# Optimization experiments

Measured on AMD Instinct MI355X. Metric: run time of the kernel, lower is better.

Reference implementation:

```python
import jax, jax.numpy as jnp
import numpy as np

N_NODES = 100000
N_EDGES = 1600000
IN_FEATS = 128
HIDDEN = 128


def _graph_conv(x, W, b, src, dst, n_nodes):
    # DGL GraphConv with norm='both': out = D_in^{-1/2} * A^T * (D_out^{-1/2} * x) @ W + b
    ones = jnp.ones((src.shape[0],), dtype=x.dtype)
    deg_out = jax.ops.segment_sum(ones, src, num_segments=n_nodes)
    deg_in = jax.ops.segment_sum(ones, dst, num_segments=n_nodes)
    norm_src = jax.lax.rsqrt(jnp.clip(deg_out, 1.0))  # [N]
    norm_dst = jax.lax.rsqrt(jnp.clip(deg_in, 1.0))   # [N]
    h = x @ W                                          # [N, F_out]
    msg = h[src] * norm_src[src][:, None]              # gather by edge src: [E, F_out]
    agg = jax.ops.segment_sum(msg, dst, num_segments=n_nodes)  # scatter-add to dst
    return agg * norm_dst[:, None] + b


def setup_inputs() -> dict:
    key = jax.random.key(0)
    ks = jax.random.split(key, 9)
    x = jax.random.normal(ks[0], (N_NODES, IN_FEATS), dtype=jnp.float32)
    src = jax.random.randint(ks[1], (N_EDGES,), 0, N_NODES, dtype=jnp.int32)
    dst = jax.random.randint(ks[2], (N_EDGES,), 0, N_NODES, dtype=jnp.int32)
    s1 = 1.0 / np.sqrt(IN_FEATS)
    s2 = 1.0 / np.sqrt(HIDDEN)
    W1 = jax.random.uniform(ks[3], (IN_FEATS, HIDDEN), jnp.float32, -s1, s1)
    b1 = jnp.zeros((HIDDEN,), jnp.float32)
    W2 = jax.random.uniform(ks[4], (HIDDEN, HIDDEN), jnp.float32, -s2, s2)
    b2 = jnp.zeros((HIDDEN,), jnp.float32)
    sp = 1.0 / np.sqrt(2 * HIDDEN)
    Wp = jax.random.uniform(ks[5], (2 * HIDDEN, 1), jnp.float32, -sp, sp)
    bp = jax.random.uniform(ks[6], (1,), jnp.float32, -sp, sp)
    return {"x": x, "W1": W1, "b1": b1, "W2": W2, "b2": b2,
            "Wp": Wp, "bp": bp, "src": src, "dst": dst}


def reference(x, W1, b1, W2, b2, Wp, bp, src, dst):
    n_nodes = x.shape[0]
    h = _graph_conv(x, W1, b1, src, dst, n_nodes)
    h = jax.nn.relu(h)
    h = _graph_conv(h, W2, b2, src, dst, n_nodes)  # final node embeddings [N, H]
    # predict_links on the same edge list: cat(h[u], h[v]) -> linear -> sigmoid
    edge_h = jnp.concatenate([h[src], h[dst]], axis=1)  # [E, 2H]
    scores = jax.nn.sigmoid(edge_h @ Wp + bp)           # [E, 1]
    return scores
```

## Files before the change

kernel.cpp:

```cpp
#include <hip/hip_runtime.h>
#include <cstdint>
#include <cstddef>

#define NN 100000
#define NE 1600000
#define F  128
#define NPAD 100352
#define NBUCK 782
#define BCAPG 2560
#define CHUNK 3125

typedef __attribute__((ext_vector_type(8))) short bf16x8;
typedef __attribute__((ext_vector_type(4))) float f32x4;

__device__ __forceinline__ unsigned short f2bf(float f) {
    unsigned u = __float_as_uint(f);
    unsigned r = (u + 0x7fffu + ((u >> 16) & 1u)) >> 16;
    return (unsigned short)r;
}
__device__ __forceinline__ void acc_bf8s(const uint4 v, const float ns, float* acc) {
    acc[0] += __uint_as_float(v.x << 16) * ns;
    acc[1] += __uint_as_float(v.x & 0xffff0000u) * ns;
    acc[2] += __uint_as_float(v.y << 16) * ns;
    acc[3] += __uint_as_float(v.y & 0xffff0000u) * ns;
    acc[4] += __uint_as_float(v.z << 16) * ns;
    acc[5] += __uint_as_float(v.z & 0xffff0000u) * ns;
    acc[6] += __uint_as_float(v.w << 16) * ns;
    acc[7] += __uint_as_float(v.w & 0xffff0000u) * ns;
}
__device__ __forceinline__ float deg2norm(int d) {
    return rsqrtf((float)max(d, 1));
}

__global__ void setup_kernel(const float* __restrict__ W2, const float* __restrict__ Wp,
                             const float* __restrict__ b2, const float* __restrict__ bp,
                             float* __restrict__ consts, float2* __restrict__ V) {
    const int tid = threadIdx.x;
    if (tid < 128) {
        float sa = 0.f, sc = 0.f;
        #pragma unroll 8
        for (int j = 0; j < F; ++j) {
            const float w = W2[tid * F + j];
            sa += w * Wp[j];
            sc += w * Wp[F + j];
        }
        V[tid] = make_float2(sa, sc);
    } else if (tid < 192) {
        const int l = tid - 128;
        const float2 bb = *(const float2*)&b2[2 * l];
        const float2 wa = *(const float2*)&Wp[2 * l];
        const float2 wc = *(const float2*)&Wp[F + 2 * l];
        float s = bb.x * (wa.x + wc.x) + bb.y * (wa.y + wc.y);
        #pragma unroll
        for (int m = 32; m > 0; m >>= 1) s += __shfl_xor(s, m);
        if (l == 0) consts[0] = s + bp[0];
    }
}

__global__ __launch_bounds__(256, 3)
void gemm1_fill_kernel(const float* __restrict__ in, const float* __restrict__ W,
                       unsigned short* __restrict__ out_bf,
                       const int* __restrict__ src, const int* __restrict__ dst,
                       int* __restrict__ deg_out, int* __restrict__ gCur,
                       int* __restrict__ srcPart) {
    __shared__ __align__(16) char smem[25008];

    const int g = blockIdx.x;
    const int r3 = g % 3;
    const int tid = threadIdx.x;

    if (r3 != 0) {
        int* packedL = (int*)smem;
        unsigned short* bktL = (unsigned short*)(packedL + CHUNK);
        int* hist = (int*)(smem + 18752);
        int* curL = hist + NBUCK;
        const int fid = (g / 3) * 2 + (r3 - 1);
        const int e0 = fid * CHUNK;
        const int nCh = min(CHUNK, NE - e0);
        for (int i = tid; i < NBUCK; i += 256) hist[i] = 0;
        __syncthreads();
        for (int i = tid; i < nCh; i += 256) {
            const int s = src[e0 + i];
            const int d = dst[e0 + i];
            atomicAdd(&deg_out[s], 1);
            const int bkt = d >> 7;
            atomicAdd(&hist[bkt], 1);
            packedL[i] = s | ((d & 127) << 17);
            bktL[i] = (unsigned short)bkt;
        }
        __syncthreads();
        for (int b = tid; b < NBUCK; b += 256) {
            const int c = hist[b];
            curL[b] = (c > 0) ? (b * BCAPG + atomicAdd(&gCur[b], c)) : 0;
        }
        __syncthreads();
        for (int i = tid; i < nCh; i += 256) {
            const int bkt = bktL[i];
            const int p = atomicAdd(&curL[bkt], 1);
            if (p < (bkt + 1) * BCAPG)
                srcPart[p] = packedL[i];
        }
        return;
    }

    char* A_s = smem;

    const int gid  = g / 3;
    const int w    = tid >> 6;
    const int lane = tid & 63;
    const int ml   = lane & 15;
    const int quad = lane >> 4;

    bf16x8 Bf[4][2];
    #pragma unroll
    for (int kb = 0; kb < 4; ++kb) {
        #pragma unroll
        for (int nb = 0; nb < 2; ++nb) {
            const int n = 32 * w + nb * 16 + ml;
            const int k0 = kb * 32 + quad * 8;
            #pragma unroll
            for (int j = 0; j < 8; ++j)
                Bf[kb][nb][j] = (short)f2bf(W[(k0 + j) * F + n]);
        }
    }

    const int nTiles = NN / 32;
    for (int tile = gid; tile < nTiles; tile += 256) {
        const int row0 = tile * 32;
        __syncthreads();
        #pragma unroll
        for (int c = 0; c < 2; ++c) {
            const int i2 = tid + 256 * c;
            const int m  = i2 >> 4;
            const int o  = i2 & 15;
            const float* xr = &in[(size_t)(row0 + m) * F + o * 8];
            const float4 v0 = *(const float4*)xr;
            const float4 v1 = *(const float4*)(xr + 4);
            short h8[8];
            h8[0] = (short)f2bf(v0.x); h8[1] = (short)f2bf(v0.y);
            h8[2] = (short)f2bf(v0.z); h8[3] = (short)f2bf(v0.w);
            h8[4] = (short)f2bf(v1.x); h8[5] = (short)f2bf(v1.y);
            h8[6] = (short)f2bf(v1.z); h8[7] = (short)f2bf(v1.w);
            const int kb2 = o >> 2, q2 = o & 3, ml2 = m & 15, mh2 = m >> 4;
            const int fo = (((mh2 * 4 + kb2) * 64) + q2 * 16 + ml2) * 16;
            *(bf16x8*)(A_s + fo) = *(bf16x8*)h8;
        }
        __syncthreads();

        f32x4 acc00 = {0,0,0,0}, acc01 = {0,0,0,0}, acc10 = {0,0,0,0}, acc11 = {0,0,0,0};
        #pragma unroll
        for (int kb = 0; kb < 4; ++kb) {
            const bf16x8 ah0 = *(const bf16x8*)(A_s + (kb * 64 + lane) * 16);
            const bf16x8 ah1 = *(const bf16x8*)(A_s + ((4 + kb) * 64 + lane) * 16);
            acc00 = __builtin_amdgcn_mfma_f32_16x16x32_bf16(ah0, Bf[kb][0], acc00, 0, 0, 0);
            acc01 = __builtin_amdgcn_mfma_f32_16x16x32_bf16(ah0, Bf[kb][1], acc01, 0, 0, 0);
            acc10 = __builtin_amdgcn_mfma_f32_16x16x32_bf16(ah1, Bf[kb][0], acc10, 0, 0, 0);
            acc11 = __builtin_amdgcn_mfma_f32_16x16x32_bf16(ah1, Bf[kb][1], acc11, 0, 0, 0);
        }

        #pragma unroll
        for (int mh = 0; mh < 2; ++mh) {
            #pragma unroll
            for (int nb = 0; nb < 2; ++nb) {
                const f32x4 a = (mh == 0) ? (nb == 0 ? acc00 : acc01)
                                          : (nb == 0 ? acc10 : acc11);
                const int row = row0 + mh * 16 + quad * 4;
                const int col = 32 * w + nb * 16 + ml;
                #pragma unroll
                for (int r = 0; r < 4; ++r)
                    out_bf[(size_t)(row + r) * F + col] = f2bf(a[r]);
            }
        }
    }
}

__global__ __launch_bounds__(256)
void gather_sort_kernel(const unsigned short* __restrict__ hs,
                        int* __restrict__ srcPart, const int* __restrict__ gCur,
                        const int* __restrict__ deg_out, const float* __restrict__ bias,
                        const float2* __restrict__ V, float2* __restrict__ uw,
                        int* __restrict__ offs, int* __restrict__ ends,
                        float* __restrict__ norm_dst) {
    __shared__ int cnt[128];
    __shared__ int loc[128];
    __shared__ int cur[128];
    __shared__ int sortedL[BCAPG];

    const int b   = blockIdx.x;
    const int tid = threadIdx.x;
    const int nlo = b * 128;
    const int nCnt = min(128, NN - nlo);
    const int eBase = b * BCAPG;
    const int total = min(gCur[b], BCAPG);

    if (tid < 128) cnt[tid] = 0;
    __syncthreads();
    for (int i = tid; i < total; i += 256)
        atomicAdd(&cnt[(srcPart[eBase + i] >> 17) & 127], 1);
    __syncthreads();
    if (tid < 128) loc[tid] = cnt[tid];
    __syncthreads();
    for (int off = 1; off < 128; off <<= 1) {
        int v = 0;
        if (tid < 128 && tid >= off) v = loc[tid - off];
        __syncthreads();
        if (tid < 128) loc[tid] += v;
        __syncthreads();
    }
    if (tid < 128) cur[tid] = loc[tid] - cnt[tid];
    if (tid < nCnt) {
        const int st = eBase + loc[tid] - cnt[tid];
        offs[nlo + tid] = st;
        ends[nlo + tid] = st + cnt[tid];
        norm_dst[nlo + tid] = deg2norm(cnt[tid]);
    }
    __syncthreads();
    for (int i = tid; i < total; i += 256) {
        const int v = srcPart[eBase + i];
        const int r = atomicAdd(&cur[(v >> 17) & 127], 1);
        sortedL[r] = v & 0x1FFFF;
    }
    __syncthreads();
    for (int i = tid; i < total; i += 256)
        srcPart[eBase + i] = sortedL[i];

    const int w  = tid >> 6;
    const int l  = tid & 63;
    const int q  = l >> 4;
    const int c8 = (l & 15) * 8;
    float bb[8];
    *(float4*)&bb[0] = *(const float4*)&bias[c8];
    *(float4*)&bb[4] = *(const float4*)&bias[c8 + 4];
    float2 Vl[8];
    #pragma unroll
    for (int k = 0; k < 8; ++k) Vl[k] = V[c8 + k];

    const int nhEnd = min((w + 1) * 32, nCnt);
    for (int nh = w * 32; nh < nhEnd; ++nh) {
        const int end = loc[nh];
        const int beg = end - cnt[nh];
        float acc[8] = {0.f, 0.f, 0.f, 0.f, 0.f, 0.f, 0.f, 0.f};
        int j = beg;
        for (; j + 16 <= end; j += 16) {
            const int s0 = sortedL[j + q];
            const int s1 = sortedL[j + 4 + q];
            const int s2 = sortedL[j + 8 + q];
            const int s3 = sortedL[j + 12 + q];
            const float ns0 = deg2norm(deg_out[s0]);
            const float ns1 = deg2norm(deg_out[s1]);
            const float ns2 = deg2norm(deg_out[s2]);
            const float ns3 = deg2norm(deg_out[s3]);
            const uint4 v0 = *(const uint4*)&hs[(size_t)s0 * F + c8];
            const uint4 v1 = *(const uint4*)&hs[(size_t)s1 * F + c8];
            const uint4 v2 = *(const uint4*)&hs[(size_t)s2 * F + c8];
            const uint4 v3 = *(const uint4*)&hs[(size_t)s3 * F + c8];
            acc_bf8s(v0, ns0, acc);
            acc_bf8s(v1, ns1, acc);
            acc_bf8s(v2, ns2, acc);
            acc_bf8s(v3, ns3, acc);
        }
        for (; j + 8 <= end; j += 8) {
            const int s0 = sortedL[j + q];
            const int s1 = sortedL[j + 4 + q];
            const float ns0 = deg2norm(deg_out[s0]);
            const float ns1 = deg2norm(deg_out[s1]);
            const uint4 v0 = *(const uint4*)&hs[(size_t)s0 * F + c8];
            const uint4 v1 = *(const uint4*)&hs[(size_t)s1 * F + c8];
            acc_bf8s(v0, ns0, acc);
            acc_bf8s(v1, ns1, acc);
        }
        for (; j + 4 <= end; j += 4) {
            const int s = sortedL[j + q];
            const float ns = deg2norm(deg_out[s]);
            const uint4 v = *(const uint4*)&hs[(size_t)s * F + c8];
            acc_bf8s(v, ns, acc);
        }
        if (j + q < end) {
            const int s = sortedL[j + q];
            const float ns = deg2norm(deg_out[s]);
            const uint4 v = *(const uint4*)&hs[(size_t)s * F + c8];
            acc_bf8s(v, ns, acc);
        }
        #pragma unroll
        for (int k = 0; k < 8; ++k) {
            acc[k] += __shfl_xor(acc[k], 16);
            acc[k] += __shfl_xor(acc[k], 32);
        }

        const int n = nlo + nh;
        const float nd = deg2norm(cnt[nh]);
        float pa = 0.f, pc = 0.f;
        #pragma unroll
        for (int k = 0; k < 8; ++k) {
            const float ok = fmaxf(acc[k] * nd + bb[k], 0.f);
            pa += ok * Vl[k].x;
            pc += ok * Vl[k].y;
        }
        #pragma unroll
        for (int m = 1; m <= 8; m <<= 1) {
            pa += __shfl_xor(pa, m);
            pc += __shfl_xor(pc, m);
        }
        if (l == 0) {
            const float ns = deg2norm(deg_out[n]);
            uw[n] = make_float2(ns * pa, ns * pc);
        }
    }
}

__global__ void ac_kernel(const float2* __restrict__ uw, const int* __restrict__ sorted_src,
                          const int* __restrict__ offs, const int* __restrict__ ends,
                          const float* __restrict__ norm_dst,
                          float* __restrict__ A, float* __restrict__ C, int nN) {
    const int gid = blockIdx.x * blockDim.x + threadIdx.x;
    const int n   = gid >> 3;
    if (n >= nN) return;
    const int sub = gid & 7;
    const int beg = offs[n];
    const int end = ends[n];
    float su = 0.f, sw = 0.f;
    for (int j = beg + sub; j < end; j += 8) {
        const float2 t = uw[sorted_src[j]];
        su += t.x;
        sw += t.y;
    }
    su += __shfl_xor(su, 1); sw += __shfl_xor(sw, 1);
    su += __shfl_xor(su, 2); sw += __shfl_xor(sw, 2);
    su += __shfl_xor(su, 4); sw += __shfl_xor(sw, 4);
    if (sub == 0) {
        const float nd = norm_dst[n];
        A[n] = nd * su;
        C[n] = nd * sw;
    }
}

__global__ void score_kernel(const float* __restrict__ A, const float* __restrict__ C,
                             const int4* __restrict__ src4, const int4* __restrict__ dst4,
                             const float* __restrict__ consts, float4* __restrict__ out4,
                             int nE4) {
    const int i = blockIdx.x * blockDim.x + threadIdx.x;
    if (i < nE4) {
        const int4 s = src4[i];
        const int4 d = dst4[i];
        const float cc = consts[0];
        float4 o;
        o.x = 1.f / (1.f + __expf(-(A[s.x] + C[d.x] + cc)));
        o.y = 1.f / (1.f + __expf(-(A[s.y] + C[d.y] + cc)));
        o.z = 1.f / (1.f + __expf(-(A[s.z] + C[d.z] + cc)));
        o.w = 1.f / (1.f + __expf(-(A[s.w] + C[d.w] + cc)));
        out4[i] = o;
    }
}

extern "C" void kernel_launch(void* const* d_in, const int* in_sizes, int n_in,
                              void* d_out, int out_size, void* d_ws, size_t ws_size,
                              hipStream_t stream) {
    const float* x  = (const float*)d_in[0];
    const float* W1 = (const float*)d_in[1];
    const float* b1 = (const float*)d_in[2];
    const float* W2 = (const float*)d_in[3];
    const float* b2 = (const float*)d_in[4];
    const float* Wp = (const float*)d_in[5];
    const float* bp = (const float*)d_in[6];
    const int*   src = (const int*)d_in[7];
    const int*   dst = (const int*)d_in[8];
    float* out = (float*)d_out;

    float* ws        = (float*)d_ws;
    float* bufA      = ws;
    int*   gCur      = (int*)(ws + NPAD);
    float* bufC      = ws + NPAD + 1024;
    float* norm_dst  = bufC + NPAD;
    int*   offs      = (int*)(norm_dst + NPAD);
    int*   ends      = offs + NPAD;
    float* consts    = (float*)(ends + NPAD);
    float2* V        = (float2*)(consts + 16);
    float2* uw       = V + 128;
    int*   srcPart   = (int*)(uw + NN);
    unsigned short* hs_bf = (unsigned short*)(srcPart + (size_t)NBUCK * BCAPG);

    hipMemsetAsync(bufA, 0, (NPAD + 1024) * sizeof(int), stream);
    setup_kernel<<<1, 256, 0, stream>>>(W2, Wp, b2, bp, consts, V);

    gemm1_fill_kernel<<<768, 256, 0, stream>>>(x, W1, hs_bf, src, dst,
                                               (int*)bufA, gCur, srcPart);

    gather_sort_kernel<<<NBUCK, 256, 0, stream>>>(hs_bf, srcPart, gCur, (const int*)bufA, b1,
                                                  V, uw, offs, ends, norm_dst);

    ac_kernel<<<(NN * 8 + 255) / 256, 256, 0, stream>>>(uw, srcPart, offs, ends, norm_dst,
                                                        bufA, bufC, NN);

    score_kernel<<<(NE / 4 + 255) / 256, 256, 0, stream>>>(bufA, bufC, (const int4*)src,
                                                           (const int4*)dst, consts,
                                                           (float4*)out, NE / 4);
}
```

Measured before the change: 312.9 us.

## Aggregate raw bf16 features first, then apply W1 GEMM per destination bucket

Reorders layer 1 so neighbour features are aggregated before the W1 multiply: the first kernel now only casts x to bf16 (plus edge bucketing and the setup constants, merged in as extra blocks). The gather kernel stages the aggregated 128 rows per bucket in shared memory and runs the MFMA GEMM with W1 there before the fused ReLU/projection. This removes the separate GEMM pass and one kernel launch. In exchange, each gather block reloads and converts W1 from global memory and uses 32KB more LDS, which may lower occupancy.

```diff
diff --git a/kernel.cpp b/kernel.cpp
--- a/kernel.cpp
+++ b/kernel.cpp
@@ -8,7 +8,8 @@
 #define NPAD 100352
 #define NBUCK 782
 #define BCAPG 2560
-#define CHUNK 3125
+#define FILLB 1024
+#define CHUNK 1563
 
 typedef __attribute__((ext_vector_type(8))) short bf16x8;
 typedef __attribute__((ext_vector_type(4))) float f32x4;
@@ -32,159 +33,112 @@
     return rsqrtf((float)max(d, 1));
 }
 
-__global__ void setup_kernel(const float* __restrict__ W2, const float* __restrict__ Wp,
-                             const float* __restrict__ b2, const float* __restrict__ bp,
-                             float* __restrict__ consts, float2* __restrict__ V) {
+__global__ __launch_bounds__(256, 3)
+void cast_fill_kernel(const float* __restrict__ x, unsigned short* __restrict__ xb,
+                      const int* __restrict__ src, const int* __restrict__ dst,
+                      int* __restrict__ deg_out, int* __restrict__ gCur,
+                      int* __restrict__ srcPart,
+                      const float* __restrict__ W2, const float* __restrict__ Wp,
+                      const float* __restrict__ b2, const float* __restrict__ bp,
+                      float* __restrict__ consts, float2* __restrict__ V) {
+    __shared__ __align__(16) char smem[15664];
+    const int g = blockIdx.x;
     const int tid = threadIdx.x;
-    if (tid < 128) {
-        float sa = 0.f, sc = 0.f;
-        #pragma unroll 8
-        for (int j = 0; j < F; ++j) {
-            const float w = W2[tid * F + j];
-            sa += w * Wp[j];
-            sc += w * Wp[F + j];
-        }
-        V[tid] = make_float2(sa, sc);
-    } else if (tid < 192) {
-        const int l = tid - 128;
-        const float2 bb = *(const float2*)&b2[2 * l];
-        const float2 wa = *(const float2*)&Wp[2 * l];
-        const float2 wc = *(const float2*)&Wp[F + 2 * l];
-        float s = bb.x * (wa.x + wc.x) + bb.y * (wa.y + wc.y);
-        #pragma unroll
-        for (int m = 32; m > 0; m >>= 1) s += __shfl_xor(s, m);
-        if (l == 0) consts[0] = s + bp[0];
-    }
-}
-
-__global__ __launch_bounds__(256, 3)
-void gemm1_fill_kernel(const float* __restrict__ in, const float* __restrict__ W,
-                       unsigned short* __restrict__ out_bf,
-                       const int* __restrict__ src, const int* __restrict__ dst,
-                       int* __restrict__ deg_out, int* __restrict__ gCur,
-                       int* __restrict__ srcPart) {
-    __shared__ __align__(16) char smem[25008];
-
-    const int g = blockIdx.x;
-    const int r3 = g % 3;
-    const int tid = threadIdx.x;
-
-    if (r3 != 0) {
-        int* packedL = (int*)smem;
-        unsigned short* bktL = (unsigned short*)(packedL + CHUNK);
-        int* hist = (int*)(smem + 18752);
-        int* curL = hist + NBUCK;
-        const int fid = (g / 3) * 2 + (r3 - 1);
-        const int e0 = fid * CHUNK;
-        const int nCh = min(CHUNK, NE - e0);
-        for (int i = tid; i < NBUCK; i += 256) hist[i] = 0;
-        __syncthreads();
-        for (int i = tid; i < nCh; i += 256) {
-            const int s = src[e0 + i];
-            const int d = dst[e0 + i];
-            atomicAdd(&deg_out[s], 1);
-            const int bkt = d >> 7;
-            atomicAdd(&hist[bkt], 1);
-            packedL[i] = s | ((d & 127) << 17);
-            bktL[i] = (unsigned short)bkt;
-        }
-        __syncthreads();
-        for (int b = tid; b < NBUCK; b += 256) {
-            const int c = hist[b];
-            curL[b] = (c > 0) ? (b * BCAPG + atomicAdd(&gCur[b], c)) : 0;
-        }
-        __syncthreads();
-        for (int i = tid; i < nCh; i += 256) {
-            const int bkt = bktL[i];
-            const int p = atomicAdd(&curL[bkt], 1);
-            if (p < (bkt + 1) * BCAPG)
-                srcPart[p] = packedL[i];
+
+    if (g >= 1152) {
+        const int i = g - 1152;
+        if (i < 128) {
+            float* red = (float*)smem;
+            float pa = 0.f, pc = 0.f;
+            if (tid < 128) {
+                const float wv = W2[i * F + tid];
+                pa = wv * Wp[tid];
+                pc = wv * Wp[F + tid];
+            }
+            #pragma unroll
+            for (int m = 32; m > 0; m >>= 1) {
+                pa += __shfl_xor(pa, m);
+                pc += __shfl_xor(pc, m);
+            }
+            if (tid < 128 && (tid & 63) == 0) {
+                red[(tid >> 6) * 2]     = pa;
+                red[(tid >> 6) * 2 + 1] = pc;
+            }
+            __syncthreads();
+            if (tid == 0) V[i] = make_float2(red[0] + red[2], red[1] + red[3]);
+        } else if (tid < 64) {
+            const float2 bb = *(const float2*)&b2[2 * tid];
+            const float2 wa = *(const float2*)&Wp[2 * tid];
+            const float2 wc = *(const float2*)&Wp[F + 2 * tid];
+            float s = bb.x * (wa.x + wc.x) + bb.y * (wa.y + wc.y);
+            #pragma unroll
+            for (int m = 32; m > 0; m >>= 1) s += __shfl_xor(s, m);
+            if (tid == 0) consts[0] = s + bp[0];
         }
         return;
     }
 
-    char* A_s = smem;
-
-    const int gid  = g / 3;
-    const int w    = tid >> 6;
-    const int lane = tid & 63;
-    const int ml   = lane & 15;
-    const int quad = lane >> 4;
-
-    bf16x8 Bf[4][2];
-    #pragma unroll
-    for (int kb = 0; kb < 4; ++kb) {
-        #pragma unroll
-        for (int nb = 0; nb < 2; ++nb) {
-            const int n = 32 * w + nb * 16 + ml;
-            const int k0 = kb * 32 + quad * 8;
-            #pragma unroll
-            for (int j = 0; j < 8; ++j)
-                Bf[kb][nb][j] = (short)f2bf(W[(k0 + j) * F + n]);
-        }
-    }
-
-    const int nTiles = NN / 32;
-    for (int tile = gid; tile < nTiles; tile += 256) {
-        const int row0 = tile * 32;
-        __syncthreads();
-        #pragma unroll
-        for (int c = 0; c < 2; ++c) {
-            const int i2 = tid + 256 * c;
-            const int m  = i2 >> 4;
-            const int o  = i2 & 15;
-            const float* xr = &in[(size_t)(row0 + m) * F + o * 8];
-            const float4 v0 = *(const float4*)xr;
-            const float4 v1 = *(const float4*)(xr + 4);
+    const int r9 = g % 9;
+    if (r9 == 4) {
+        const int cb = g / 9;
+        const int total8 = NN * F / 8;
+        for (int i = cb * 256 + tid; i < total8; i += 128 * 256) {
+            const float4 v0 = *(const float4*)&x[(size_t)i * 8];
+            const float4 v1 = *(const float4*)&x[(size_t)i * 8 + 4];
             short h8[8];
             h8[0] = (short)f2bf(v0.x); h8[1] = (short)f2bf(v0.y);
             h8[2] = (short)f2bf(v0.z); h8[3] = (short)f2bf(v0.w);
             h8[4] = (short)f2bf(v1.x); h8[5] = (short)f2bf(v1.y);
             h8[6] = (short)f2bf(v1.z); h8[7] = (short)f2bf(v1.w);
-            const int kb2 = o >> 2, q2 = o & 3, ml2 = m & 15, mh2 = m >> 4;
-            const int fo = (((mh2 * 4 + kb2) * 64) + q2 * 16 + ml2) * 16;
-            *(bf16x8*)(A_s + fo) = *(bf16x8*)h8;
-        }
-        __syncthreads();
-
-        f32x4 acc00 = {0,0,0,0}, acc01 = {0,0,0,0}, acc10 = {0,0,0,0}, acc11 = {0,0,0,0};
-        #pragma unroll
-        for (int kb = 0; kb < 4; ++kb) {
-            const bf16x8 ah0 = *(const bf16x8*)(A_s + (kb * 64 + lane) * 16);
-            const bf16x8 ah1 = *(const bf16x8*)(A_s + ((4 + kb) * 64 + lane) * 16);
-            acc00 = __builtin_amdgcn_mfma_f32_16x16x32_bf16(ah0, Bf[kb][0], acc00, 0, 0, 0);
-            acc01 = __builtin_amdgcn_mfma_f32_16x16x32_bf16(ah0, Bf[kb][1], acc01, 0, 0, 0);
-            acc10 = __builtin_amdgcn_mfma_f32_16x16x32_bf16(ah1, Bf[kb][0], acc10, 0, 0, 0);
-            acc11 = __builtin_amdgcn_mfma_f32_16x16x32_bf16(ah1, Bf[kb][1], acc11, 0, 0, 0);
-        }
-
-        #pragma unroll
-        for (int mh = 0; mh < 2; ++mh) {
-            #pragma unroll
-            for (int nb = 0; nb < 2; ++nb) {
-                const f32x4 a = (mh == 0) ? (nb == 0 ? acc00 : acc01)
-                                          : (nb == 0 ? acc10 : acc11);
-                const int row = row0 + mh * 16 + quad * 4;
-                const int col = 32 * w + nb * 16 + ml;
-                #pragma unroll
-                for (int r = 0; r < 4; ++r)
-                    out_bf[(size_t)(row + r) * F + col] = f2bf(a[r]);
-            }
-        }
+            *(bf16x8*)&xb[(size_t)i * 8] = *(bf16x8*)h8;
+        }
+        return;
+    }
+
+    int* packedL = (int*)smem;
+    unsigned short* bktL = (unsigned short*)(packedL + CHUNK);
+    int* hist = (int*)(smem + 9380);
+    int* curL = hist + NBUCK;
+    const int fid = (g / 9) * 8 + (r9 > 4 ? r9 - 1 : r9);
+    const int e0 = fid * CHUNK;
+    const int nCh = min(CHUNK, NE - e0);
+    for (int i = tid; i < NBUCK; i += 256) hist[i] = 0;
+    __syncthreads();
+    for (int i = tid; i < nCh; i += 256) {
+        const int s = src[e0 + i];
+        const int d = dst[e0 + i];
+        atomicAdd(&deg_out[s], 1);
+        const int bkt = d >> 7;
+        atomicAdd(&hist[bkt], 1);
+        packedL[i] = s | ((d & 127) << 17);
+        bktL[i] = (unsigned short)bkt;
+    }
+    __syncthreads();
+    for (int b = tid; b < NBUCK; b += 256) {
+        const int c = hist[b];
+        curL[b] = (c > 0) ? (b * BCAPG + atomicAdd(&gCur[b], c)) : 0;
+    }
+    __syncthreads();
+    for (int i = tid; i < nCh; i += 256) {
+        const int bkt = bktL[i];
+        const int p = atomicAdd(&curL[bkt], 1);
+        if (p < (bkt + 1) * BCAPG)
+            srcPart[p] = packedL[i];
     }
 }
 
 __global__ __launch_bounds__(256)
-void gather_sort_kernel(const unsigned short* __restrict__ hs,
+void gather_gemm_kernel(const unsigned short* __restrict__ xb,
                         int* __restrict__ srcPart, const int* __restrict__ gCur,
-                        const int* __restrict__ deg_out, const float* __restrict__ bias,
-                        const float2* __restrict__ V, float2* __restrict__ uw,
-                        int* __restrict__ offs, int* __restrict__ ends,
-                        float* __restrict__ norm_dst) {
+                        const int* __restrict__ deg_out, const float* __restrict__ W1,
+                        const float* __restrict__ b1, const float2* __restrict__ V,
+                        float2* __restrict__ uw, int* __restrict__ offs,
+                        int* __restrict__ ends, float* __restrict__ norm_dst) {
     __shared__ int cnt[128];
     __shared__ int loc[128];
     __shared__ int cur[128];
     __shared__ int sortedL[BCAPG];
+    __shared__ __align__(16) char gS[32768];
 
     const int b   = blockIdx.x;
     const int tid = threadIdx.x;
@@ -224,16 +178,11 @@
     for (int i = tid; i < total; i += 256)
         srcPart[eBase + i] = sortedL[i];
 
-    const int w  = tid >> 6;
-    const int l  = tid & 63;
-    const int q  = l >> 4;
-    const int c8 = (l & 15) * 8;
-    float bb[8];
-    *(float4*)&bb[0] = *(const float4*)&bias[c8];
-    *(float4*)&bb[4] = *(const float4*)&bias[c8 + 4];
-    float2 Vl[8];
-    #pragma unroll
-    for (int k = 0; k < 8; ++k) Vl[k] = V[c8 + k];
+    const int w    = tid >> 6;
+    const int lane = tid & 63;
+    const int q    = lane >> 4;
+    const int ml   = lane & 15;
+    const int c8   = ml * 8;
 
     const int nhEnd = min((w + 1) * 32, nCnt);
     for (int nh = w * 32; nh < nhEnd; ++nh) {
@@ -250,10 +199,10 @@
             const float ns1 = deg2norm(deg_out[s1]);
             const float ns2 = deg2norm(deg_out[s2]);
             const float ns3 = deg2norm(deg_out[s3]);
-            const uint4 v0 = *(const uint4*)&hs[(size_t)s0 * F + c8];
-            const uint4 v1 = *(const uint4*)&hs[(size_t)s1 * F + c8];
-            const uint4 v2 = *(const uint4*)&hs[(size_t)s2 * F + c8];
-            const uint4 v3 = *(const uint4*)&hs[(size_t)s3 * F + c8];
+            const uint4 v0 = *(const uint4*)&xb[(size_t)s0 * F + c8];
+            const uint4 v1 = *(const uint4*)&xb[(size_t)s1 * F + c8];
+            const uint4 v2 = *(const uint4*)&xb[(size_t)s2 * F + c8];
+            const uint4 v3 = *(const uint4*)&xb[(size_t)s3 * F + c8];
             acc_bf8s(v0, ns0, acc);
             acc_bf8s(v1, ns1, acc);
             acc_bf8s(v2, ns2, acc);
@@ -264,21 +213,21 @@
             const int s1 = sortedL[j + 4 + q];
             const float ns0 = deg2norm(deg_out[s0]);
             const float ns1 = deg2norm(deg_out[s1]);
-            const uint4 v0 = *(const uint4*)&hs[(size_t)s0 * F + c8];
-            const uint4 v1 = *(const uint4*)&hs[(size_t)s1 * F + c8];
+            const uint4 v0 = *(const uint4*)&xb[(size_t)s0 * F + c8];
+            const uint4 v1 = *(const uint4*)&xb[(size_t)s1 * F + c8];
             acc_bf8s(v0, ns0, acc);
             acc_bf8s(v1, ns1, acc);
         }
         for (; j + 4 <= end; j += 4) {
             const int s = sortedL[j + q];
             const float ns = deg2norm(deg_out[s]);
-            const uint4 v = *(const uint4*)&hs[(size_t)s * F + c8];
+            const uint4 v = *(const uint4*)&xb[(size_t)s * F + c8];
             acc_bf8s(v, ns, acc);
         }
         if (j + q < end) {
             const int s = sortedL[j + q];
             const float ns = deg2norm(deg_out[s]);
-            const uint4 v = *(const uint4*)&hs[(size_t)s * F + c8];
+            const uint4 v = *(const uint4*)&xb[(size_t)s * F + c8];
             acc_bf8s(v, ns, acc);
         }
         #pragma unroll
@@ -286,24 +235,69 @@
             acc[k] += __shfl_xor(acc[k], 16);
             acc[k] += __shfl_xor(acc[k], 32);
         }
-
-        const int n = nlo + nh;
-        const float nd = deg2norm(cnt[nh]);
-        float pa = 0.f, pc = 0.f;
+        if (q == 0) {
+            short h8[8];
+            #pragma unroll
+            for (int k = 0; k < 8; ++k) h8[k] = (short)f2bf(acc[k]);
+            const int kb2 = ml >> 2, q2 = ml & 3, ml2 = nh & 15, mh2 = nh >> 4;
+            *(bf16x8*)(gS + (((mh2 * 4 + kb2) * 64) + q2 * 16 + ml2) * 16) = *(bf16x8*)h8;
+        }
+    }
+    __syncthreads();
+
+    f32x4 oa[2][8];
+    #pragma unroll
+    for (int mh = 0; mh < 2; ++mh)
         #pragma unroll
-        for (int k = 0; k < 8; ++k) {
-            const float ok = fmaxf(acc[k] * nd + bb[k], 0.f);
-            pa += ok * Vl[k].x;
-            pc += ok * Vl[k].y;
-        }
+        for (int nb = 0; nb < 8; ++nb) oa[mh][nb] = (f32x4){0.f, 0.f, 0.f, 0.f};
+
+    #pragma unroll
+    for (int kb = 0; kb < 4; ++kb) {
+        const bf16x8 a0 = *(const bf16x8*)(gS + ((((2 * w + 0) * 4 + kb) * 64) + lane) * 16);
+        const bf16x8 a1 = *(const bf16x8*)(gS + ((((2 * w + 1) * 4 + kb) * 64) + lane) * 16);
+        const int k0 = kb * 32 + q * 8;
         #pragma unroll
-        for (int m = 1; m <= 8; m <<= 1) {
-            pa += __shfl_xor(pa, m);
-            pc += __shfl_xor(pc, m);
-        }
-        if (l == 0) {
-            const float ns = deg2norm(deg_out[n]);
-            uw[n] = make_float2(ns * pa, ns * pc);
+        for (int nb = 0; nb < 8; ++nb) {
+            const int ncol = nb * 16 + ml;
+            short bf8a[8];
+            #pragma unroll
+            for (int j = 0; j < 8; ++j)
+                bf8a[j] = (short)f2bf(W1[(k0 + j) * F + ncol]);
+            const bf16x8 bf = *(bf16x8*)bf8a;
+            oa[0][nb] = __builtin_amdgcn_mfma_f32_16x16x32_bf16(a0, bf, oa[0][nb], 0, 0, 0);
+            oa[1][nb] = __builtin_amdgcn_mfma_f32_16x16x32_bf16(a1, bf, oa[1][nb], 0, 0, 0);
+        }
+    }
+
+    float b1v[8]; float2 Vv[8];
+    #pragma unroll
+    for (int nb = 0; nb < 8; ++nb) {
+        b1v[nb] = b1[nb * 16 + ml];
+        Vv[nb]  = V[nb * 16 + ml];
+    }
+    #pragma unroll
+    for (int mh = 0; mh < 2; ++mh) {
+        #pragma unroll
+        for (int r = 0; r < 4; ++r) {
+            const int row = 32 * w + mh * 16 + q * 4 + r;
+            const float nd = deg2norm(cnt[row]);
+            float pa = 0.f, pc = 0.f;
+            #pragma unroll
+            for (int nb = 0; nb < 8; ++nb) {
+                const float ok = fmaxf(oa[mh][nb][r] * nd + b1v[nb], 0.f);
+                pa += ok * Vv[nb].x;
+                pc += ok * Vv[nb].y;
+            }
+            #pragma unroll
+            for (int m = 1; m <= 8; m <<= 1) {
+                pa += __shfl_xor(pa, m);
+                pc += __shfl_xor(pc, m);
+            }
+            if (ml == 0 && row < nCnt) {
+                const int n = nlo + row;
+                const float ns = deg2norm(deg_out[n]);
+                uw[n] = make_float2(ns * pa, ns * pc);
+            }
         }
     }
 }
@@ -377,16 +371,15 @@
     float2* V        = (float2*)(consts + 16);
     float2* uw       = V + 128;
     int*   srcPart   = (int*)(uw + NN);
-    unsigned short* hs_bf = (unsigned short*)(srcPart + (size_t)NBUCK * BCAPG);
+    unsigned short* xb = (unsigned short*)(srcPart + (size_t)NBUCK * BCAPG);
 
     hipMemsetAsync(bufA, 0, (NPAD + 1024) * sizeof(int), stream);
-    setup_kernel<<<1, 256, 0, stream>>>(W2, Wp, b2, bp, consts, V);
-
-    gemm1_fill_kernel<<<768, 256, 0, stream>>>(x, W1, hs_bf, src, dst,
-                                               (int*)bufA, gCur, srcPart);
-
-    gather_sort_kernel<<<NBUCK, 256, 0, stream>>>(hs_bf, srcPart, gCur, (const int*)bufA, b1,
-                                                  V, uw, offs, ends, norm_dst);
+
+    cast_fill_kernel<<<1281, 256, 0, stream>>>(x, xb, src, dst, (int*)bufA, gCur, srcPart,
+                                               W2, Wp, b2, bp, consts, V);
+
+    gather_gemm_kernel<<<NBUCK, 256, 0, stream>>>(xb, srcPart, gCur, (const int*)bufA,
+                                                  W1, b1, V, uw, offs, ends, norm_dst);
 
     ac_kernel<<<(NN * 8 + 255) / 256, 256, 0, stream>>>(uw, srcPart, offs, ends, norm_dst,
                                                         bufA, bufC, NN);
```

Measured after the change: 372.6 us. 1.19x slower.
